# Performance work log

Hardware: AMD Instinct MI355X
Metric: run time of the kernel (lower is better)

Reference implementation:

```python
import math
import jax, jax.numpy as jnp
import numpy as np

SQ, SK, B, D = 2048, 2048, 4, 512


def setup_inputs() -> dict:
    key = jax.random.key(0)
    kq, kk, kv = jax.random.split(key, 3)
    Q = jax.random.normal(kq, (SQ, B, D), dtype=jnp.float32)
    K = jax.random.normal(kk, (SK, B, D), dtype=jnp.float32)
    V = jax.random.normal(kv, (SK, B, D), dtype=jnp.float32)
    key_mask = jnp.zeros((SK, B), dtype=bool)  # True = masked key
    return {"Q": Q, "K": K, "V": V, "key_mask": key_mask}


def reference(Q, K, V, key_mask):
    # Layout: [seq, batch, d]. scores: [Sq, B, Sk]
    d = K.shape[2]
    scores = jnp.einsum('ibd,kbd->ibk', Q, K) / math.sqrt(d)
    Sq, Bb, Sk = scores.shape
    # causal mask: disallow k > i
    causal = jnp.triu(jnp.ones((Sq, Sk), dtype=bool), k=1)[:, None, :]
    neg_inf = jnp.array(-jnp.inf, dtype=scores.dtype)
    scores = jnp.where(causal, neg_inf, scores)
    # key padding mask: key_mask [Sk, B] -> [1, B, Sk]
    scores = jnp.where(key_mask.T[None, :, :], neg_inf, scores)
    p = jax.nn.softmax(scores, axis=2)
    return jnp.einsum('ibk,kbd->ibd', p, V)
```

## Files before the change

### kernel.cpp

```cpp
#include <hip/hip_runtime.h>

#define SEQ   2048
#define BATCH 4
#define DIM   512
#define POFF  65536
#define LDS_TOTAL 67584
#define NEG_INF  (-__builtin_inff())

typedef short short8 __attribute__((ext_vector_type(8)));
typedef float floatx4 __attribute__((ext_vector_type(4)));

using lds_char = __attribute__((address_space(3))) char;
using g_void   = const __attribute__((address_space(1))) void;
using l_void   = __attribute__((address_space(3))) void;

__device__ __forceinline__ short to_bf16(float x){
    unsigned u = __float_as_uint(x);
    unsigned r = (u + 0x7fffu + ((u >> 16) & 1u)) >> 16;
    return (short)r;
}

__device__ __forceinline__ short8 pack8f(floatx4 a, floatx4 b, float s){
    short8 r;
    r[0]=to_bf16(a[0]*s); r[1]=to_bf16(a[1]*s); r[2]=to_bf16(a[2]*s); r[3]=to_bf16(a[3]*s);
    r[4]=to_bf16(b[0]*s); r[5]=to_bf16(b[1]*s); r[6]=to_bf16(b[2]*s); r[7]=to_bf16(b[3]*s);
    return r;
}

extern "C" __global__ void __launch_bounds__(256)
conv_k(const float* __restrict__ K, short* __restrict__ Kimg)
{
    const int t    = blockIdx.x * 256 + threadIdx.x;
    const int d8   = t & 63;
    const int row  = t >> 6;
    const int k    = row >> 2;
    const int b    = row & 3;
    const float* src = K + (size_t)row * DIM + d8 * 8;
    floatx4 f0 = *(const floatx4*)src;
    floatx4 f1 = *(const floatx4*)(src + 4);
    const int slot = (d8 * 8) ^ ((k & 7) << 3);
    *(short8*)(Kimg + ((size_t)b * SEQ + k) * DIM + slot) = pack8f(f0, f1, 1.0f);
}

extern "C" __global__ void __launch_bounds__(256)
conv_v(const float* __restrict__ V, short* __restrict__ Vt)
{
    const int t    = blockIdx.x * 256 + threadIdx.x;
    const int dv   = t & 511;
    const int rest = t >> 9;
    const int kc   = rest & 255;
    const int b    = rest >> 8;
    short8 colv;
    #pragma unroll
    for (int i = 0; i < 8; ++i){
        const float f = V[((size_t)(kc*8 + i) * BATCH + b) * DIM + dv];
        colv[i] = to_bf16(f);
    }
    *(short8*)(Vt + ((size_t)b * DIM + dv) * SEQ + kc * 8) = colv;
}

extern "C" __global__ void __launch_bounds__(256)
merge_o(const float* __restrict__ partO, const float* __restrict__ stats,
        float* __restrict__ Og)
{
    const int t = blockIdx.x * 256 + threadIdx.x;
    const int d = t & 511;
    const int uu = t >> 9;
    const int b = uu & 3;
    const int v = uu >> 2;
    const int v16 = v >> 4;
    const int r   = v & 15;
    const int p0  = (v16*4 + b)*2;
    const float O0 = partO[((size_t)p0*16 + r)*512 + d];
    const float O1 = partO[((size_t)(p0+1)*16 + r)*512 + d];
    const float m0 = stats[p0*32 + r],     l0 = stats[p0*32 + 16 + r];
    const float m1 = stats[(p0+1)*32 + r], l1 = stats[(p0+1)*32 + 16 + r];
    const float M  = fmaxf(m0, m1);
    const float a0 = (m0 == NEG_INF) ? 0.f : __expf(m0 - M);
    const float a1 = (m1 == NEG_INF) ? 0.f : __expf(m1 - M);
    const float l  = a0*l0 + a1*l1;
    const float inv = (l > 0.f) ? 1.0f/l : 0.f;
    Og[((size_t)v*BATCH + b)*DIM + d] = (a0*O0 + a1*O1) * inv;
}

extern "C" __global__ void __launch_bounds__(256, 2)
fa_fwd(const float* __restrict__ Qg, const short* __restrict__ Kb,
       const short* __restrict__ Vt, const unsigned char* __restrict__ Mg,
       float* __restrict__ partO, float* __restrict__ stats)
{
    extern __shared__ __align__(16) char smem[];
    const int tid  = threadIdx.x;
    const int w    = tid >> 6;
    const int lane = tid & 63;
    const int g    = lane >> 4;
    const int c    = lane & 15;

    const int slot = blockIdx.x & 7;
    const int b    = slot >> 1;
    const int h    = slot & 1;
    const int idx  = blockIdx.x >> 3;
    const int u    = idx & 1;
    const int s    = idx >> 1;

    const int cntA  = (s + 2 - h) >> 1;
    const int cntB  = (65 - s - h) >> 1;
    const int total = cntA + cntB;

    const short* Kbb = Kb + (size_t)b * SEQ * DIM;
    const short* Vtb = Vt + (size_t)b * DIM * SEQ;
    char* Pb = smem + POFF;

    #define STAGE(tt, dd) { \
        const short* ksrc_ = Kbb + ((size_t)((tt)*32 + w*8)) * DIM + lane*8; \
        char* dst_ = smem + (dd)*32768 + w*8192; \
        _Pragma("unroll") \
        for (int i2 = 0; i2 < 8; ++i2) \
            __builtin_amdgcn_global_load_lds((g_void*)(ksrc_ + (size_t)i2*DIM), \
                (l_void*)(lds_char*)(dst_ + i2*1024), 16, 0, 0); }

    #define TILE_OF(j) ((j) < cntA ? (h + 2*(j)) : (h + 2*((j) - cntA)))

    const float scale = 0.04419417382415922f;
    short8 qreg[16];
    floatx4 oacc[8];
    float mrow[4], lrow[4];
    int qt_cur = s;

    {
        const float* qrow = Qg + ((size_t)((s*2+u)*16 + c) * BATCH + b) * DIM + g * 8;
        #pragma unroll
        for (int ks = 0; ks < 16; ++ks){
            floatx4 f0 = *(const floatx4*)(qrow + ks*32);
            floatx4 f1 = *(const floatx4*)(qrow + ks*32 + 4);
            qreg[ks] = pack8f(f0, f1, scale);
        }
    }
    #pragma unroll
    for (int i=0;i<8;++i){ floatx4 z = {0.f,0.f,0.f,0.f}; oacc[i]=z; }
    #pragma unroll
    for (int jj=0;jj<4;++jj){ mrow[jj] = NEG_INF; lrow[jj] = 0.f; }

    STAGE(TILE_OF(0), 0);

    #pragma unroll 1
    for (int j = 0; j < total; ++j){

        if (j == cntA){
            const int inst = ((s*2 + u)*4 + b)*2 + h;
            float* po = partO + (size_t)inst * 16 * 512;
            #pragma unroll
            for (int nt = 0; nt < 8; ++nt){
                #pragma unroll
                for (int jj = 0; jj < 4; ++jj)
                    po[(size_t)(g*4 + jj)*512 + w*128 + nt*16 + c] = oacc[nt][jj];
            }
            if (w == 0 && c == 0){
                #pragma unroll
                for (int jj = 0; jj < 4; ++jj){
                    stats[inst*32 + g*4 + jj]      = mrow[jj];
                    stats[inst*32 + 16 + g*4 + jj] = lrow[jj];
                }
            }
            qt_cur = 63 - s;
            const float* qrow = Qg + ((size_t)((qt_cur*2+u)*16 + c) * BATCH + b) * DIM + g * 8;
            #pragma unroll
            for (int ks = 0; ks < 16; ++ks){
                floatx4 f0 = *(const floatx4*)(qrow + ks*32);
                floatx4 f1 = *(const floatx4*)(qrow + ks*32 + 4);
                qreg[ks] = pack8f(f0, f1, scale);
            }
            #pragma unroll
            for (int i=0;i<8;++i){ floatx4 z = {0.f,0.f,0.f,0.f}; oacc[i]=z; }
            #pragma unroll
            for (int jj=0;jj<4;++jj){ mrow[jj] = NEG_INF; lrow[jj] = 0.f; }
        }

        const int d     = j & 1;
        const int kb    = TILE_OF(j) * 32;
        const int qrow0 = (qt_cur*2 + u) * 16;

        asm volatile("s_waitcnt vmcnt(0)" ::: "memory");
        __syncthreads();

        if (j + 1 < total) STAGE(TILE_OF(j+1), d ^ 1);

        const char* kb_ = smem + d*32768;

        const unsigned char km0 = Mg[(kb + c) * BATCH + b];
        const unsigned char km1 = Mg[(kb + 16 + c) * BATCH + b];

        short8 vf[8];
        #pragma unroll
        for (int nt = 0; nt < 8; ++nt){
            const int dv = w*128 + nt*16 + c;
            vf[nt] = *(const short8*)(Vtb + (size_t)dv * SEQ + kb + g*8);
        }

        floatx4 sacc[2];
        { floatx4 z = {0.f,0.f,0.f,0.f}; sacc[0]=z; sacc[1]=z; }
        #pragma unroll
        for (int ks = 0; ks < 16; ++ks){
            #pragma unroll
            for (int jcol = 0; jcol < 2; ++jcol){
                short8 kf = *(const short8*)(kb_ + jcol*16384 + c*1024 +
                               ((ks*64 + g*16) ^ ((c & 7) << 4)));
                sacc[jcol] = __builtin_amdgcn_mfma_f32_16x16x32_bf16(qreg[ks], kf, sacc[jcol], 0,0,0);
            }
        }

        float sv[2][4];
        #pragma unroll
        for (int jcol = 0; jcol < 2; ++jcol){
            const int col = kb + jcol*16 + c;
            const unsigned char km = jcol ? km1 : km0;
            #pragma unroll
            for (int jj = 0; jj < 4; ++jj){
                const int row = qrow0 + g*4 + jj;
                sv[jcol][jj] = (col > row || km) ? NEG_INF : sacc[jcol][jj];
            }
        }
        float pmax[4];
        #pragma unroll
        for (int jj=0;jj<4;++jj) pmax[jj] = fmaxf(sv[0][jj], sv[1][jj]);
        #pragma unroll
        for (int msk=1; msk<16; msk<<=1){
            #pragma unroll
            for (int jj=0;jj<4;++jj)
                pmax[jj] = fmaxf(pmax[jj], __shfl_xor(pmax[jj], msk, 64));
        }
        const bool okd = (pmax[0] <= mrow[0]+8.f) && (pmax[1] <= mrow[1]+8.f)
                      && (pmax[2] <= mrow[2]+8.f) && (pmax[3] <= mrow[3]+8.f);
        if (!__all(okd)){
            float fsc[4];
            #pragma unroll
            for (int jj=0;jj<4;++jj){
                const float M = fmaxf(mrow[jj], pmax[jj]);
                const float f = (mrow[jj] == NEG_INF) ? 0.f : __expf(mrow[jj] - M);
                mrow[jj] = M; lrow[jj] *= f; fsc[jj] = f;
            }
            #pragma unroll
            for (int nt=0; nt<8; ++nt){
                #pragma unroll
                for (int jj=0; jj<4; ++jj) oacc[nt][jj] *= fsc[jj];
            }
        }
        float parr[2][4], psum[4] = {0.f,0.f,0.f,0.f};
        #pragma unroll
        for (int jcol=0; jcol<2; ++jcol){
            #pragma unroll
            for (int jj=0; jj<4; ++jj){
                const float x = sv[jcol][jj];
                const float e = (x == NEG_INF) ? 0.f : __expf(x - mrow[jj]);
                parr[jcol][jj] = e; psum[jj] += e;
            }
        }
        #pragma unroll
        for (int msk=1; msk<16; msk<<=1){
            #pragma unroll
            for (int jj=0;jj<4;++jj) psum[jj] += __shfl_xor(psum[jj], msk, 64);
        }
        #pragma unroll
        for (int jj=0;jj<4;++jj) lrow[jj] += psum[jj];

        #pragma unroll
        for (int jcol=0; jcol<2; ++jcol){
            #pragma unroll
            for (int jj=0; jj<4; ++jj)
                *(short*)(Pb + (g*4 + jj)*64 + (jcol*16 + c)*2) = to_bf16(parr[jcol][jj]);
        }

        const short8 pfrag = *(const short8*)(Pb + c*64 + g*16);
        #pragma unroll
        for (int nt = 0; nt < 8; ++nt){
            oacc[nt] = __builtin_amdgcn_mfma_f32_16x16x32_bf16(pfrag, vf[nt], oacc[nt], 0,0,0);
        }
    }

    {
        const int inst = ((qt_cur*2 + u)*4 + b)*2 + h;
        float* po = partO + (size_t)inst * 16 * 512;
        #pragma unroll
        for (int nt = 0; nt < 8; ++nt){
            #pragma unroll
            for (int jj = 0; jj < 4; ++jj)
                po[(size_t)(g*4 + jj)*512 + w*128 + nt*16 + c] = oacc[nt][jj];
        }
        if (w == 0 && c == 0){
            #pragma unroll
            for (int jj = 0; jj < 4; ++jj){
                stats[inst*32 + g*4 + jj]      = mrow[jj];
                stats[inst*32 + 16 + g*4 + jj] = lrow[jj];
            }
        }
    }
    #undef STAGE
    #undef TILE_OF
}

extern "C" void kernel_launch(void* const* d_in, const int* in_sizes, int n_in,
                              void* d_out, int out_size, void* d_ws, size_t ws_size,
                              hipStream_t stream)
{
    const float* Q = (const float*)d_in[0];
    const float* K = (const float*)d_in[1];
    const float* V = (const float*)d_in[2];
    const unsigned char* M = (const unsigned char*)d_in[3];
    float* O = (float*)d_out;
    (void)in_sizes; (void)n_in; (void)out_size; (void)ws_size;

    short* Kb    = (short*)d_ws;
    short* Vt    = Kb + (size_t)BATCH * SEQ * DIM;
    float* partO = (float*)(Vt + (size_t)BATCH * SEQ * DIM);
    float* stats = partO + (size_t)1024 * 16 * 512;

    conv_k<<<2048, 256, 0, stream>>>(K, Kb);
    conv_v<<<2048, 256, 0, stream>>>(V, Vt);

    hipFuncSetAttribute(reinterpret_cast<const void*>(fa_fwd),
                        hipFuncAttributeMaxDynamicSharedMemorySize, LDS_TOTAL);
    fa_fwd<<<512, 256, LDS_TOTAL, stream>>>(Q, Kb, Vt, M, partO, stats);

    merge_o<<<16384, 256, 0, stream>>>(partO, stats, O);
}
```

Baseline: 141.1 us.

## Split KV range four ways, single-buffer K tile, store bf16 partial outputs

Each query tile's key range is now split across four blocks instead of two, doubling the grid to 1024 blocks and raising the occupancy hint to 4 blocks per CU. The K tile in LDS goes from double to single buffering, with an extra barrier before the next tile is staged, which halves LDS use so more blocks fit on a CU. Partial outputs are written as packed bf16 and the merge kernel combines four partials. The aim is better CU utilisation and less partial-output traffic, at the cost of losing load/compute overlap on K, twice as many partials to merge, and some precision loss in the partials.

```diff
diff --git a/kernel.cpp b/kernel.cpp
--- a/kernel.cpp
+++ b/kernel.cpp
@@ -3,8 +3,8 @@
 #define SEQ   2048
 #define BATCH 4
 #define DIM   512
-#define POFF  65536
-#define LDS_TOTAL 67584
+#define POFF  32768
+#define LDS_TOTAL 34816
 #define NEG_INF  (-__builtin_inff())
 
 typedef short short8 __attribute__((ext_vector_type(8)));
@@ -18,6 +18,11 @@
     unsigned u = __float_as_uint(x);
     unsigned r = (u + 0x7fffu + ((u >> 16) & 1u)) >> 16;
     return (short)r;
+}
+
+__device__ __forceinline__ float from_bf16(short s){
+    unsigned u = ((unsigned)(unsigned short)s) << 16;
+    return __uint_as_float(u);
 }
 
 __device__ __forceinline__ short8 pack8f(floatx4 a, floatx4 b, float s){
@@ -60,7 +65,7 @@
 }
 
 extern "C" __global__ void __launch_bounds__(256)
-merge_o(const float* __restrict__ partO, const float* __restrict__ stats,
+merge_o(const short* __restrict__ partO, const float* __restrict__ stats,
         float* __restrict__ Og)
 {
     const int t = blockIdx.x * 256 + threadIdx.x;
@@ -70,23 +75,30 @@
     const int v = uu >> 2;
     const int v16 = v >> 4;
     const int r   = v & 15;
-    const int p0  = (v16*4 + b)*2;
-    const float O0 = partO[((size_t)p0*16 + r)*512 + d];
-    const float O1 = partO[((size_t)(p0+1)*16 + r)*512 + d];
-    const float m0 = stats[p0*32 + r],     l0 = stats[p0*32 + 16 + r];
-    const float m1 = stats[(p0+1)*32 + r], l1 = stats[(p0+1)*32 + 16 + r];
-    const float M  = fmaxf(m0, m1);
-    const float a0 = (m0 == NEG_INF) ? 0.f : __expf(m0 - M);
-    const float a1 = (m1 == NEG_INF) ? 0.f : __expf(m1 - M);
-    const float l  = a0*l0 + a1*l1;
-    const float inv = (l > 0.f) ? 1.0f/l : 0.f;
-    Og[((size_t)v*BATCH + b)*DIM + d] = (a0*O0 + a1*O1) * inv;
-}
-
-extern "C" __global__ void __launch_bounds__(256, 2)
+    const int p0  = (v16*4 + b)*4;
+    float m[4], l[4], o[4];
+    #pragma unroll
+    for (int h = 0; h < 4; ++h){
+        m[h] = stats[(p0+h)*32 + r];
+        l[h] = stats[(p0+h)*32 + 16 + r];
+        o[h] = from_bf16(partO[((size_t)(p0+h)*16 + r)*512 + d]);
+    }
+    const float M = fmaxf(fmaxf(m[0], m[1]), fmaxf(m[2], m[3]));
+    float lsum = 0.f, osum = 0.f;
+    #pragma unroll
+    for (int h = 0; h < 4; ++h){
+        const float a = (m[h] == NEG_INF) ? 0.f : __expf(m[h] - M);
+        lsum += a * l[h];
+        osum += a * o[h];
+    }
+    const float inv = (lsum > 0.f) ? 1.0f/lsum : 0.f;
+    Og[((size_t)v*BATCH + b)*DIM + d] = osum * inv;
+}
+
+extern "C" __global__ void __launch_bounds__(256, 4)
 fa_fwd(const float* __restrict__ Qg, const short* __restrict__ Kb,
        const short* __restrict__ Vt, const unsigned char* __restrict__ Mg,
-       float* __restrict__ partO, float* __restrict__ stats)
+       short* __restrict__ partO, float* __restrict__ stats)
 {
     extern __shared__ __align__(16) char smem[];
     const int tid  = threadIdx.x;
@@ -97,28 +109,50 @@
 
     const int slot = blockIdx.x & 7;
     const int b    = slot >> 1;
-    const int h    = slot & 1;
+    const int hlo  = slot & 1;
     const int idx  = blockIdx.x >> 3;
     const int u    = idx & 1;
-    const int s    = idx >> 1;
-
-    const int cntA  = (s + 2 - h) >> 1;
-    const int cntB  = (65 - s - h) >> 1;
+    const int hhi  = (idx >> 1) & 1;
+    const int s    = idx >> 2;
+    const int h    = hhi*2 + hlo;
+
+    const int cntA  = (s >= h) ? (((s - h) >> 2) + 1) : 0;
+    const int cntB  = ((63 - s - h) >> 2) + 1;
     const int total = cntA + cntB;
 
     const short* Kbb = Kb + (size_t)b * SEQ * DIM;
     const short* Vtb = Vt + (size_t)b * DIM * SEQ;
     char* Pb = smem + POFF;
 
-    #define STAGE(tt, dd) { \
+    #define STAGE(tt) { \
         const short* ksrc_ = Kbb + ((size_t)((tt)*32 + w*8)) * DIM + lane*8; \
-        char* dst_ = smem + (dd)*32768 + w*8192; \
+        char* dst_ = smem + w*8192; \
         _Pragma("unroll") \
         for (int i2 = 0; i2 < 8; ++i2) \
             __builtin_amdgcn_global_load_lds((g_void*)(ksrc_ + (size_t)i2*DIM), \
                 (l_void*)(lds_char*)(dst_ + i2*1024), 16, 0, 0); }
 
-    #define TILE_OF(j) ((j) < cntA ? (h + 2*(j)) : (h + 2*((j) - cntA)))
+    #define TILE_OF(j) ((j) < cntA ? (h + 4*(j)) : (h + 4*((j) - cntA)))
+
+    #define FINALIZE(qtv) { \
+        const int inst = (((qtv)*2 + u)*4 + b)*4 + h; \
+        short* po = partO + (size_t)inst * 16 * 512; \
+        _Pragma("unroll") \
+        for (int nt = 0; nt < 8; ++nt){ \
+            _Pragma("unroll") \
+            for (int jj = 0; jj < 4; ++jj){ \
+                const float v0 = oacc[nt][jj]; \
+                const float v1 = __shfl_xor(v0, 1, 64); \
+                if (!(c & 1)){ \
+                    const unsigned pk = (unsigned)(unsigned short)to_bf16(v0) \
+                                      | ((unsigned)(unsigned short)to_bf16(v1) << 16); \
+                    *(unsigned*)(po + (size_t)(g*4 + jj)*512 + w*128 + nt*16 + c) = pk; \
+                } } } \
+        if (w == 0 && c == 0){ \
+            _Pragma("unroll") \
+            for (int jj = 0; jj < 4; ++jj){ \
+                stats[inst*32 + g*4 + jj]      = mrow[jj]; \
+                stats[inst*32 + 16 + g*4 + jj] = lrow[jj]; } } }
 
     const float scale = 0.04419417382415922f;
     short8 qreg[16];
@@ -140,27 +174,13 @@
     #pragma unroll
     for (int jj=0;jj<4;++jj){ mrow[jj] = NEG_INF; lrow[jj] = 0.f; }
 
-    STAGE(TILE_OF(0), 0);
+    STAGE(TILE_OF(0));
 
     #pragma unroll 1
     for (int j = 0; j < total; ++j){
 
         if (j == cntA){
-            const int inst = ((s*2 + u)*4 + b)*2 + h;
-            float* po = partO + (size_t)inst * 16 * 512;
-            #pragma unroll
-            for (int nt = 0; nt < 8; ++nt){
-                #pragma unroll
-                for (int jj = 0; jj < 4; ++jj)
-                    po[(size_t)(g*4 + jj)*512 + w*128 + nt*16 + c] = oacc[nt][jj];
-            }
-            if (w == 0 && c == 0){
-                #pragma unroll
-                for (int jj = 0; jj < 4; ++jj){
-                    stats[inst*32 + g*4 + jj]      = mrow[jj];
-                    stats[inst*32 + 16 + g*4 + jj] = lrow[jj];
-                }
-            }
+            FINALIZE(s);
             qt_cur = 63 - s;
             const float* qrow = Qg + ((size_t)((qt_cur*2+u)*16 + c) * BATCH + b) * DIM + g * 8;
             #pragma unroll
@@ -175,16 +195,11 @@
             for (int jj=0;jj<4;++jj){ mrow[jj] = NEG_INF; lrow[jj] = 0.f; }
         }
 
-        const int d     = j & 1;
         const int kb    = TILE_OF(j) * 32;
         const int qrow0 = (qt_cur*2 + u) * 16;
 
         asm volatile("s_waitcnt vmcnt(0)" ::: "memory");
         __syncthreads();
-
-        if (j + 1 < total) STAGE(TILE_OF(j+1), d ^ 1);
-
-        const char* kb_ = smem + d*32768;
 
         const unsigned char km0 = Mg[(kb + c) * BATCH + b];
         const unsigned char km1 = Mg[(kb + 16 + c) * BATCH + b];
@@ -202,11 +217,15 @@
         for (int ks = 0; ks < 16; ++ks){
             #pragma unroll
             for (int jcol = 0; jcol < 2; ++jcol){
-                short8 kf = *(const short8*)(kb_ + jcol*16384 + c*1024 +
+                short8 kf = *(const short8*)(smem + jcol*16384 + c*1024 +
                                ((ks*64 + g*16) ^ ((c & 7) << 4)));
                 sacc[jcol] = __builtin_amdgcn_mfma_f32_16x16x32_bf16(qreg[ks], kf, sacc[jcol], 0,0,0);
             }
         }
+
+        __syncthreads();
+
+        if (j + 1 < total) STAGE(TILE_OF(j+1));
 
         float sv[2][4];
         #pragma unroll
@@ -276,25 +295,11 @@
         }
     }
 
-    {
-        const int inst = ((qt_cur*2 + u)*4 + b)*2 + h;
-        float* po = partO + (size_t)inst * 16 * 512;
-        #pragma unroll
-        for (int nt = 0; nt < 8; ++nt){
-            #pragma unroll
-            for (int jj = 0; jj < 4; ++jj)
-                po[(size_t)(g*4 + jj)*512 + w*128 + nt*16 + c] = oacc[nt][jj];
-        }
-        if (w == 0 && c == 0){
-            #pragma unroll
-            for (int jj = 0; jj < 4; ++jj){
-                stats[inst*32 + g*4 + jj]      = mrow[jj];
-                stats[inst*32 + 16 + g*4 + jj] = lrow[jj];
-            }
-        }
-    }
+    FINALIZE(qt_cur);
+
     #undef STAGE
     #undef TILE_OF
+    #undef FINALIZE
 }
 
 extern "C" void kernel_launch(void* const* d_in, const int* in_sizes, int n_in,
@@ -310,15 +315,15 @@
 
     short* Kb    = (short*)d_ws;
     short* Vt    = Kb + (size_t)BATCH * SEQ * DIM;
-    float* partO = (float*)(Vt + (size_t)BATCH * SEQ * DIM);
-    float* stats = partO + (size_t)1024 * 16 * 512;
+    short* partO = Vt + (size_t)BATCH * SEQ * DIM;
+    float* stats = (float*)(partO + (size_t)2048 * 16 * 512);
 
     conv_k<<<2048, 256, 0, stream>>>(K, Kb);
     conv_v<<<2048, 256, 0, stream>>>(V, Vt);
 
     hipFuncSetAttribute(reinterpret_cast<const void*>(fa_fwd),
                         hipFuncAttributeMaxDynamicSharedMemorySize, LDS_TOTAL);
-    fa_fwd<<<512, 256, LDS_TOTAL, stream>>>(Q, Kb, Vt, M, partO, stats);
+    fa_fwd<<<1024, 256, LDS_TOTAL, stream>>>(Q, Kb, Vt, M, partO, stats);
 
     merge_o<<<16384, 256, 0, stream>>>(partO, stats, O);
 }
```

Result: slower. 300.5 us (+112.9%).

## Share 64-key K tiles across both query halves in 512-thread attention blocks

Applied to the files above, without the earlier changes.

The attention kernel now uses 512-thread blocks. The two 16-row query halves share each staged K tile, and the tile width grows from 32 to 64 keys, so K is loaded into LDS once per block instead of once per query half. The softmax row sum is now accumulated with an MFMA against a vector of ones instead of cross-lane shuffle reductions, and each wave writes P into its own swizzled LDS buffer. The K and V conversion kernels are merged into one launch. LDS use per block grows to about 144 KB, so only one block fits per CU, and each thread holds more registers for V fragments.

```diff
diff --git a/kernel.cpp b/kernel.cpp
--- a/kernel.cpp
+++ b/kernel.cpp
@@ -3,8 +3,8 @@
 #define SEQ   2048
 #define BATCH 4
 #define DIM   512
-#define POFF  65536
-#define LDS_TOTAL 67584
+#define PAOFF 131072
+#define LDS_TOTAL 147456
 #define NEG_INF  (-__builtin_inff())
 
 typedef short short8 __attribute__((ext_vector_type(8)));
@@ -28,35 +28,35 @@
 }
 
 extern "C" __global__ void __launch_bounds__(256)
-conv_k(const float* __restrict__ K, short* __restrict__ Kimg)
+conv_kv(const float* __restrict__ K, const float* __restrict__ V,
+        short* __restrict__ Kimg, short* __restrict__ Vt)
 {
-    const int t    = blockIdx.x * 256 + threadIdx.x;
-    const int d8   = t & 63;
-    const int row  = t >> 6;
-    const int k    = row >> 2;
-    const int b    = row & 3;
-    const float* src = K + (size_t)row * DIM + d8 * 8;
-    floatx4 f0 = *(const floatx4*)src;
-    floatx4 f1 = *(const floatx4*)(src + 4);
-    const int slot = (d8 * 8) ^ ((k & 7) << 3);
-    *(short8*)(Kimg + ((size_t)b * SEQ + k) * DIM + slot) = pack8f(f0, f1, 1.0f);
-}
-
-extern "C" __global__ void __launch_bounds__(256)
-conv_v(const float* __restrict__ V, short* __restrict__ Vt)
-{
-    const int t    = blockIdx.x * 256 + threadIdx.x;
-    const int dv   = t & 511;
-    const int rest = t >> 9;
-    const int kc   = rest & 255;
-    const int b    = rest >> 8;
-    short8 colv;
-    #pragma unroll
-    for (int i = 0; i < 8; ++i){
-        const float f = V[((size_t)(kc*8 + i) * BATCH + b) * DIM + dv];
-        colv[i] = to_bf16(f);
+    const int bid = blockIdx.x;
+    if (bid < 2048){
+        const int t    = bid * 256 + threadIdx.x;
+        const int d8   = t & 63;
+        const int row  = t >> 6;
+        const int k    = row >> 2;
+        const int b    = row & 3;
+        const float* src = K + (size_t)row * DIM + d8 * 8;
+        floatx4 f0 = *(const floatx4*)src;
+        floatx4 f1 = *(const floatx4*)(src + 4);
+        const int slot = (d8 * 8) ^ ((k & 7) << 3);
+        *(short8*)(Kimg + ((size_t)b * SEQ + k) * DIM + slot) = pack8f(f0, f1, 1.0f);
+    } else {
+        const int t    = (bid - 2048) * 256 + threadIdx.x;
+        const int dv   = t & 511;
+        const int rest = t >> 9;
+        const int kc   = rest & 255;
+        const int b    = rest >> 8;
+        short8 colv;
+        #pragma unroll
+        for (int i = 0; i < 8; ++i){
+            const float f = V[((size_t)(kc*8 + i) * BATCH + b) * DIM + dv];
+            colv[i] = to_bf16(f);
+        }
+        *(short8*)(Vt + ((size_t)b * DIM + dv) * SEQ + kc * 8) = colv;
     }
-    *(short8*)(Vt + ((size_t)b * DIM + dv) * SEQ + kc * 8) = colv;
 }
 
 extern "C" __global__ void __launch_bounds__(256)
@@ -83,7 +83,7 @@
     Og[((size_t)v*BATCH + b)*DIM + d] = (a0*O0 + a1*O1) * inv;
 }
 
-extern "C" __global__ void __launch_bounds__(256, 2)
+extern "C" __global__ void __launch_bounds__(512, 2)
 fa_fwd(const float* __restrict__ Qg, const short* __restrict__ Kb,
        const short* __restrict__ Vt, const unsigned char* __restrict__ Mg,
        float* __restrict__ partO, float* __restrict__ stats)
@@ -94,25 +94,27 @@
     const int lane = tid & 63;
     const int g    = lane >> 4;
     const int c    = lane & 15;
+    const int qhalf = w & 1;
+    const int dvq   = w >> 1;
 
     const int slot = blockIdx.x & 7;
     const int b    = slot >> 1;
     const int h    = slot & 1;
-    const int idx  = blockIdx.x >> 3;
-    const int u    = idx & 1;
-    const int s    = idx >> 1;
-
-    const int cntA  = (s + 2 - h) >> 1;
-    const int cntB  = (65 - s - h) >> 1;
+    const int s    = blockIdx.x >> 3;
+
+    const int TA = (s + 2) >> 1;
+    const int TB = (65 - s) >> 1;
+    const int cntA  = (TA - h + 1) >> 1;
+    const int cntB  = (TB - h + 1) >> 1;
     const int total = cntA + cntB;
 
     const short* Kbb = Kb + (size_t)b * SEQ * DIM;
     const short* Vtb = Vt + (size_t)b * DIM * SEQ;
-    char* Pb = smem + POFF;
+    char* Pb = smem + PAOFF + w*2048;
 
     #define STAGE(tt, dd) { \
-        const short* ksrc_ = Kbb + ((size_t)((tt)*32 + w*8)) * DIM + lane*8; \
-        char* dst_ = smem + (dd)*32768 + w*8192; \
+        const short* ksrc_ = Kbb + ((size_t)((tt)*64 + w*8)) * DIM + lane*8; \
+        char* dst_ = smem + (dd)*65536 + w*8192; \
         _Pragma("unroll") \
         for (int i2 = 0; i2 < 8; ++i2) \
             __builtin_amdgcn_global_load_lds((g_void*)(ksrc_ + (size_t)i2*DIM), \
@@ -120,14 +122,33 @@
 
     #define TILE_OF(j) ((j) < cntA ? (h + 2*(j)) : (h + 2*((j) - cntA)))
 
+    #define FINALIZE(qtv) { \
+        const int inst = (((qtv)*2 + qhalf)*4 + b)*2 + h; \
+        float* po = partO + (size_t)inst * 16 * 512; \
+        _Pragma("unroll") \
+        for (int nt = 0; nt < 8; ++nt){ \
+            _Pragma("unroll") \
+            for (int jj = 0; jj < 4; ++jj) \
+                po[(size_t)(g*4 + jj)*512 + dvq*128 + nt*16 + c] = oacc[nt][jj]; } \
+        if (dvq == 0 && c == 0){ \
+            _Pragma("unroll") \
+            for (int jj = 0; jj < 4; ++jj){ \
+                stats[inst*32 + g*4 + jj]      = mrow[jj]; \
+                stats[inst*32 + 16 + g*4 + jj] = lacc[jj]; } } }
+
     const float scale = 0.04419417382415922f;
+    short8 ones;
+    #pragma unroll
+    for (int i = 0; i < 8; ++i) ones[i] = (short)0x3F80;
+
     short8 qreg[16];
     floatx4 oacc[8];
-    float mrow[4], lrow[4];
+    floatx4 lacc;
+    float mrow[4];
     int qt_cur = s;
 
     {
-        const float* qrow = Qg + ((size_t)((s*2+u)*16 + c) * BATCH + b) * DIM + g * 8;
+        const float* qrow = Qg + ((size_t)((s*2+qhalf)*16 + c) * BATCH + b) * DIM + g * 8;
         #pragma unroll
         for (int ks = 0; ks < 16; ++ks){
             floatx4 f0 = *(const floatx4*)(qrow + ks*32);
@@ -137,8 +158,9 @@
     }
     #pragma unroll
     for (int i=0;i<8;++i){ floatx4 z = {0.f,0.f,0.f,0.f}; oacc[i]=z; }
+    { floatx4 z = {0.f,0.f,0.f,0.f}; lacc = z; }
     #pragma unroll
-    for (int jj=0;jj<4;++jj){ mrow[jj] = NEG_INF; lrow[jj] = 0.f; }
+    for (int jj=0;jj<4;++jj) mrow[jj] = NEG_INF;
 
     STAGE(TILE_OF(0), 0);
 
@@ -146,23 +168,9 @@
     for (int j = 0; j < total; ++j){
 
         if (j == cntA){
-            const int inst = ((s*2 + u)*4 + b)*2 + h;
-            float* po = partO + (size_t)inst * 16 * 512;
-            #pragma unroll
-            for (int nt = 0; nt < 8; ++nt){
-                #pragma unroll
-                for (int jj = 0; jj < 4; ++jj)
-                    po[(size_t)(g*4 + jj)*512 + w*128 + nt*16 + c] = oacc[nt][jj];
-            }
-            if (w == 0 && c == 0){
-                #pragma unroll
-                for (int jj = 0; jj < 4; ++jj){
-                    stats[inst*32 + g*4 + jj]      = mrow[jj];
-                    stats[inst*32 + 16 + g*4 + jj] = lrow[jj];
-                }
-            }
+            FINALIZE(s);
             qt_cur = 63 - s;
-            const float* qrow = Qg + ((size_t)((qt_cur*2+u)*16 + c) * BATCH + b) * DIM + g * 8;
+            const float* qrow = Qg + ((size_t)((qt_cur*2+qhalf)*16 + c) * BATCH + b) * DIM + g * 8;
             #pragma unroll
             for (int ks = 0; ks < 16; ++ks){
                 floatx4 f0 = *(const floatx4*)(qrow + ks*32);
@@ -171,57 +179,63 @@
             }
             #pragma unroll
             for (int i=0;i<8;++i){ floatx4 z = {0.f,0.f,0.f,0.f}; oacc[i]=z; }
-            #pragma unroll
-            for (int jj=0;jj<4;++jj){ mrow[jj] = NEG_INF; lrow[jj] = 0.f; }
+            { floatx4 z = {0.f,0.f,0.f,0.f}; lacc = z; }
+            #pragma unroll
+            for (int jj=0;jj<4;++jj) mrow[jj] = NEG_INF;
         }
 
         const int d     = j & 1;
-        const int kb    = TILE_OF(j) * 32;
-        const int qrow0 = (qt_cur*2 + u) * 16;
+        const int kb    = TILE_OF(j) * 64;
+        const int qrow0 = (qt_cur*2 + qhalf) * 16;
 
         asm volatile("s_waitcnt vmcnt(0)" ::: "memory");
         __syncthreads();
 
         if (j + 1 < total) STAGE(TILE_OF(j+1), d ^ 1);
 
-        const char* kb_ = smem + d*32768;
-
-        const unsigned char km0 = Mg[(kb + c) * BATCH + b];
-        const unsigned char km1 = Mg[(kb + 16 + c) * BATCH + b];
-
-        short8 vf[8];
-        #pragma unroll
-        for (int nt = 0; nt < 8; ++nt){
-            const int dv = w*128 + nt*16 + c;
-            vf[nt] = *(const short8*)(Vtb + (size_t)dv * SEQ + kb + g*8);
-        }
-
-        floatx4 sacc[2];
-        { floatx4 z = {0.f,0.f,0.f,0.f}; sacc[0]=z; sacc[1]=z; }
+        const char* kb_ = smem + d*65536;
+
+        unsigned char km[4];
+        #pragma unroll
+        for (int jc = 0; jc < 4; ++jc) km[jc] = Mg[(kb + jc*16 + c) * BATCH + b];
+
+        floatx4 sacc[4];
+        #pragma unroll
+        for (int jc=0;jc<4;++jc){ floatx4 z = {0.f,0.f,0.f,0.f}; sacc[jc]=z; }
         #pragma unroll
         for (int ks = 0; ks < 16; ++ks){
             #pragma unroll
-            for (int jcol = 0; jcol < 2; ++jcol){
-                short8 kf = *(const short8*)(kb_ + jcol*16384 + c*1024 +
+            for (int jc = 0; jc < 4; ++jc){
+                short8 kf = *(const short8*)(kb_ + (jc*16 + c)*1024 +
                                ((ks*64 + g*16) ^ ((c & 7) << 4)));
-                sacc[jcol] = __builtin_amdgcn_mfma_f32_16x16x32_bf16(qreg[ks], kf, sacc[jcol], 0,0,0);
-            }
-        }
-
-        float sv[2][4];
-        #pragma unroll
-        for (int jcol = 0; jcol < 2; ++jcol){
-            const int col = kb + jcol*16 + c;
-            const unsigned char km = jcol ? km1 : km0;
+                sacc[jc] = __builtin_amdgcn_mfma_f32_16x16x32_bf16(qreg[ks], kf, sacc[jc], 0,0,0);
+            }
+        }
+
+        short8 vf[2][8];
+        #pragma unroll
+        for (int kk = 0; kk < 2; ++kk){
+            #pragma unroll
+            for (int nt = 0; nt < 8; ++nt){
+                const int dv = dvq*128 + nt*16 + c;
+                vf[kk][nt] = *(const short8*)(Vtb + (size_t)dv * SEQ + kb + kk*32 + g*8);
+            }
+        }
+
+        float sv[4][4];
+        #pragma unroll
+        for (int jc = 0; jc < 4; ++jc){
+            const int col = kb + jc*16 + c;
             #pragma unroll
             for (int jj = 0; jj < 4; ++jj){
                 const int row = qrow0 + g*4 + jj;
-                sv[jcol][jj] = (col > row || km) ? NEG_INF : sacc[jcol][jj];
+                sv[jc][jj] = (col > row || km[jc]) ? NEG_INF : sacc[jc][jj];
             }
         }
         float pmax[4];
         #pragma unroll
-        for (int jj=0;jj<4;++jj) pmax[jj] = fmaxf(sv[0][jj], sv[1][jj]);
+        for (int jj=0;jj<4;++jj)
+            pmax[jj] = fmaxf(fmaxf(sv[0][jj], sv[1][jj]), fmaxf(sv[2][jj], sv[3][jj]));
         #pragma unroll
         for (int msk=1; msk<16; msk<<=1){
             #pragma unroll
@@ -236,65 +250,44 @@
             for (int jj=0;jj<4;++jj){
                 const float M = fmaxf(mrow[jj], pmax[jj]);
                 const float f = (mrow[jj] == NEG_INF) ? 0.f : __expf(mrow[jj] - M);
-                mrow[jj] = M; lrow[jj] *= f; fsc[jj] = f;
+                mrow[jj] = M; fsc[jj] = f;
             }
             #pragma unroll
             for (int nt=0; nt<8; ++nt){
                 #pragma unroll
                 for (int jj=0; jj<4; ++jj) oacc[nt][jj] *= fsc[jj];
             }
-        }
-        float parr[2][4], psum[4] = {0.f,0.f,0.f,0.f};
-        #pragma unroll
-        for (int jcol=0; jcol<2; ++jcol){
+            #pragma unroll
+            for (int jj=0; jj<4; ++jj) lacc[jj] *= fsc[jj];
+        }
+
+        #pragma unroll
+        for (int jc=0; jc<4; ++jc){
             #pragma unroll
             for (int jj=0; jj<4; ++jj){
-                const float x = sv[jcol][jj];
+                const float x = sv[jc][jj];
                 const float e = (x == NEG_INF) ? 0.f : __expf(x - mrow[jj]);
-                parr[jcol][jj] = e; psum[jj] += e;
-            }
-        }
-        #pragma unroll
-        for (int msk=1; msk<16; msk<<=1){
-            #pragma unroll
-            for (int jj=0;jj<4;++jj) psum[jj] += __shfl_xor(psum[jj], msk, 64);
-        }
-        #pragma unroll
-        for (int jj=0;jj<4;++jj) lrow[jj] += psum[jj];
-
-        #pragma unroll
-        for (int jcol=0; jcol<2; ++jcol){
-            #pragma unroll
-            for (int jj=0; jj<4; ++jj)
-                *(short*)(Pb + (g*4 + jj)*64 + (jcol*16 + c)*2) = to_bf16(parr[jcol][jj]);
-        }
-
-        const short8 pfrag = *(const short8*)(Pb + c*64 + g*16);
-        #pragma unroll
-        for (int nt = 0; nt < 8; ++nt){
-            oacc[nt] = __builtin_amdgcn_mfma_f32_16x16x32_bf16(pfrag, vf[nt], oacc[nt], 0,0,0);
+                const int r = g*4 + jj;
+                *(short*)(Pb + r*128 + (((jc*16 + c)*2) ^ ((r & 7) << 4))) = to_bf16(e);
+            }
+        }
+
+        #pragma unroll
+        for (int kk = 0; kk < 2; ++kk){
+            const short8 pfrag = *(const short8*)(Pb + c*128 +
+                                   ((kk*64 + g*16) ^ ((c & 7) << 4)));
+            #pragma unroll
+            for (int nt = 0; nt < 8; ++nt)
+                oacc[nt] = __builtin_amdgcn_mfma_f32_16x16x32_bf16(pfrag, vf[kk][nt], oacc[nt], 0,0,0);
+            lacc = __builtin_amdgcn_mfma_f32_16x16x32_bf16(pfrag, ones, lacc, 0,0,0);
         }
     }
 
-    {
-        const int inst = ((qt_cur*2 + u)*4 + b)*2 + h;
-        float* po = partO + (size_t)inst * 16 * 512;
-        #pragma unroll
-        for (int nt = 0; nt < 8; ++nt){
-            #pragma unroll
-            for (int jj = 0; jj < 4; ++jj)
-                po[(size_t)(g*4 + jj)*512 + w*128 + nt*16 + c] = oacc[nt][jj];
-        }
-        if (w == 0 && c == 0){
-            #pragma unroll
-            for (int jj = 0; jj < 4; ++jj){
-                stats[inst*32 + g*4 + jj]      = mrow[jj];
-                stats[inst*32 + 16 + g*4 + jj] = lrow[jj];
-            }
-        }
-    }
+    FINALIZE(qt_cur);
+
     #undef STAGE
     #undef TILE_OF
+    #undef FINALIZE
 }
 
 extern "C" void kernel_launch(void* const* d_in, const int* in_sizes, int n_in,
@@ -313,12 +306,11 @@
     float* partO = (float*)(Vt + (size_t)BATCH * SEQ * DIM);
     float* stats = partO + (size_t)1024 * 16 * 512;
 
-    conv_k<<<2048, 256, 0, stream>>>(K, Kb);
-    conv_v<<<2048, 256, 0, stream>>>(V, Vt);
+    conv_kv<<<4096, 256, 0, stream>>>(K, V, Kb, Vt);
 
     hipFuncSetAttribute(reinterpret_cast<const void*>(fa_fwd),
                         hipFuncAttributeMaxDynamicSharedMemorySize, LDS_TOTAL);
-    fa_fwd<<<512, 256, LDS_TOTAL, stream>>>(Q, Kb, Vt, M, partO, stats);
+    fa_fwd<<<256, 512, LDS_TOTAL, stream>>>(Q, Kb, Vt, M, partO, stats);
 
     merge_o<<<16384, 256, 0, stream>>>(partO, stats, O);
 }
```

Measured after the change: 153.8 us. 1.09x slower.
